# Kernel tuning notes

Hardware: AMD Instinct MI355X
Metric: run time of the kernel (lower is better)

## Reference

```python
import jax, jax.numpy as jnp
import numpy as np

N_EMBD = 768
N_HEAD = 12
HEAD_DIM = N_EMBD // N_HEAD  # 64


def apply_rotary_emb(x, cos, sin):
    d = x.shape[-1] // 2
    x1, x2 = x[..., :d], x[..., d:]
    y1 = x1 * cos + x2 * sin
    y2 = x1 * -sin + x2 * cos
    return jnp.concatenate([y1, y2], axis=-1)


def rms_norm(x):
    return x * jax.lax.rsqrt(jnp.mean(jnp.square(x), axis=-1, keepdims=True) + 1e-06)


def setup_inputs() -> dict:
    key = jax.random.key(0)
    ks = jax.random.split(key, 7)
    B, T = 2, 2048
    x = jax.random.normal(ks[0], (B, T, N_EMBD), dtype=jnp.float32)
    # cos/sin broadcast over (B, head) axes of [B, T, H, HEAD_DIM//2]
    cos = jax.random.uniform(ks[1], (T, 1, HEAD_DIM // 2), dtype=jnp.float32)
    sin = jax.random.uniform(ks[2], (T, 1, HEAD_DIM // 2), dtype=jnp.float32)
    scale = 1.0 / np.sqrt(N_EMBD)
    wq = jax.random.normal(ks[3], (N_EMBD, N_EMBD), dtype=jnp.float32) * scale
    wk = jax.random.normal(ks[4], (N_EMBD, N_EMBD), dtype=jnp.float32) * scale
    wv = jax.random.normal(ks[5], (N_EMBD, N_EMBD), dtype=jnp.float32) * scale
    wproj = jax.random.normal(ks[6], (N_EMBD, N_EMBD), dtype=jnp.float32) * scale
    return {"x": x, "cos": cos, "sin": sin, "wq": wq, "wk": wk, "wv": wv, "wproj": wproj}


def reference(x, cos, sin, wq, wk, wv, wproj):
    B, T, C = x.shape
    q = (x @ wq).reshape(B, T, N_HEAD, HEAD_DIM)
    k = (x @ wk).reshape(B, T, N_HEAD, HEAD_DIM)
    v = (x @ wv).reshape(B, T, N_HEAD, HEAD_DIM)
    q = rms_norm(apply_rotary_emb(q, cos, sin))
    k = rms_norm(apply_rotary_emb(k, cos, sin))
    # [B, H, T, T] attention scores (non-causal, as in source)
    attn = jnp.einsum('bqhd,bkhd->bhqk', q, k) / jnp.sqrt(jnp.float32(HEAD_DIM))
    attn = jax.nn.softmax(attn, axis=-1)
    y = jnp.einsum('bhqk,bkhd->bqhd', attn, v).reshape(B, T, C)
    return y @ wproj
```

## Files before the change

### kernel.cpp

```cpp
#include <hip/hip_runtime.h>
#include <hip/hip_bf16.h>
#include <stdint.h>

typedef __attribute__((ext_vector_type(8))) __bf16 bf16x8;
typedef __attribute__((ext_vector_type(4))) __bf16 bf16x4;
typedef __attribute__((ext_vector_type(4))) float f32x4;
typedef __attribute__((ext_vector_type(8))) unsigned short u16x8;

#define DEVI __device__ __forceinline__

DEVI void gload16(const void* g, void* l) {
  __builtin_amdgcn_global_load_lds((const __attribute__((address_space(1))) void*)g,
                                   (__attribute__((address_space(3))) void*)l, 16, 0, 0);
}

__global__ __launch_bounds__(256) void cvt_x_k(const float* __restrict__ x,
                                               __bf16* __restrict__ xb, int n4) {
  int i = blockIdx.x * blockDim.x + threadIdx.x;
  int stride = gridDim.x * blockDim.x;
  for (; i < n4; i += stride) {
    float4 v = ((const float4*)x)[i];
    bf16x4 o;
    o[0] = (__bf16)v.x; o[1] = (__bf16)v.y; o[2] = (__bf16)v.z; o[3] = (__bf16)v.w;
    ((bf16x4*)xb)[i] = o;
  }
}

__global__ __launch_bounds__(256) void wtrans_k(const float* __restrict__ wq,
                                                const float* __restrict__ wk,
                                                const float* __restrict__ wv,
                                                const float* __restrict__ wp,
                                                __bf16* __restrict__ WT) {
  __shared__ float tile[32][33];
  const float* W = (blockIdx.z == 0) ? wq : (blockIdx.z == 1) ? wk : (blockIdx.z == 2) ? wv : wp;
  int n0 = blockIdx.x * 32, k0 = blockIdx.y * 32;
  int tx = threadIdx.x, ty = threadIdx.y;
#pragma unroll
  for (int j = 0; j < 4; ++j)
    tile[ty + 8 * j][tx] = W[(size_t)(k0 + ty + 8 * j) * 768 + n0 + tx];
  __syncthreads();
#pragma unroll
  for (int j = 0; j < 4; ++j)
    WT[(size_t)(blockIdx.z * 768 + n0 + ty + 8 * j) * 768 + k0 + tx] =
        (__bf16)tile[tx][ty + 8 * j];
}

template <int EPI>
__global__ __launch_bounds__(256) void gemm_k(const __bf16* __restrict__ A,
                                              const __bf16* __restrict__ B,
                                              void* __restrict__ Cout,
                                              const float* __restrict__ cosT,
                                              const float* __restrict__ sinT,
                                              int K, int lda, int ldb, int ldc) {
  __shared__ __align__(16) __bf16 Al[128 * 32];
  __shared__ __align__(16) __bf16 Bl[128 * 32];
  const int tid = threadIdx.x, lane = tid & 63, w = tid >> 6;
  const int wm = w >> 1, wn = w & 1;
  const int m0 = blockIdx.y * 128, n0 = blockIdx.x * 128;
  const int c = lane & 15, g = lane >> 4;
  f32x4 acc[4][4] = {};

  for (int k0 = 0; k0 < K; k0 += 32) {
#pragma unroll
    for (int i = 0; i < 2; ++i) {
      int e = (i * 256 + tid) * 8;
      int row = e >> 5, col = e & 31;
      gload16(A + (size_t)(m0 + row) * lda + k0 + col, (char*)Al + 2 * (size_t)e);
      gload16(B + (size_t)(n0 + row) * ldb + k0 + col, (char*)Bl + 2 * (size_t)e);
    }
    __syncthreads();
    bf16x8 af[4], bfr[4];
#pragma unroll
    for (int q = 0; q < 4; ++q)
      af[q] = *(const bf16x8*)&Al[(wm * 64 + q * 16 + c) * 32 + 8 * g];
#pragma unroll
    for (int q = 0; q < 4; ++q)
      bfr[q] = *(const bf16x8*)&Bl[(wn * 64 + q * 16 + c) * 32 + 8 * g];
#pragma unroll
    for (int mf = 0; mf < 4; ++mf)
#pragma unroll
      for (int nf = 0; nf < 4; ++nf)
        acc[mf][nf] = __builtin_amdgcn_mfma_f32_16x16x32_bf16(af[mf], bfr[nf],
                                                              acc[mf][nf], 0, 0, 0);
    __syncthreads();
  }

  if (EPI == 1) {
    __bf16* out = (__bf16*)Cout;
    const int colbase = n0 + wn * 64;
    const int plane = colbase / 768;
#pragma unroll
    for (int mf = 0; mf < 4; ++mf) {
#pragma unroll
      for (int r = 0; r < 4; ++r) {
        int row = m0 + wm * 64 + mf * 16 + 4 * g + r;
        float v0 = acc[mf][0][r], v1 = acc[mf][1][r], v2 = acc[mf][2][r], v3 = acc[mf][3][r];
        float y0, y1, y2, y3;
        if (plane < 2) {
          int t = row & 2047;
          float c0 = cosT[t * 32 + c],      s0 = sinT[t * 32 + c];
          float c1 = cosT[t * 32 + 16 + c], s1 = sinT[t * 32 + 16 + c];
          y0 = v0 * c0 + v2 * s0;
          y2 = v2 * c0 - v0 * s0;
          y1 = v1 * c1 + v3 * s1;
          y3 = v3 * c1 - v1 * s1;
          float ss = y0 * y0 + y1 * y1 + y2 * y2 + y3 * y3;
          ss += __shfl_xor(ss, 1); ss += __shfl_xor(ss, 2);
          ss += __shfl_xor(ss, 4); ss += __shfl_xor(ss, 8);
          float rn = rsqrtf(ss * (1.0f / 64.0f) + 1e-6f);
          y0 *= rn; y1 *= rn; y2 *= rn; y3 *= rn;
        } else {
          y0 = v0; y1 = v1; y2 = v2; y3 = v3;
        }
        size_t base = (size_t)row * ldc + colbase + c;
        out[base +  0] = (__bf16)y0;
        out[base + 16] = (__bf16)y1;
        out[base + 32] = (__bf16)y2;
        out[base + 48] = (__bf16)y3;
      }
    }
  } else {
    float* out = (float*)Cout;
#pragma unroll
    for (int mf = 0; mf < 4; ++mf)
#pragma unroll
      for (int nf = 0; nf < 4; ++nf)
#pragma unroll
        for (int r = 0; r < 4; ++r) {
          int row = m0 + wm * 64 + mf * 16 + 4 * g + r;
          out[(size_t)row * ldc + n0 + wn * 64 + nf * 16 + c] = acc[mf][nf][r];
        }
  }
}

__global__ __launch_bounds__(256) void attn_k(const __bf16* __restrict__ QKV,
                                              __bf16* __restrict__ Yb) {
  constexpr int TT = 2048;
  __shared__ __align__(16) __bf16 Kl[128 * 64];
  __shared__ __align__(16) __bf16 Vl[64 * 128];
  __shared__ __align__(16) __bf16 Pl[4][16 * 136];
  const int tid = threadIdx.x, lane = tid & 63, w = tid >> 6;
  const int c = lane & 15, g = lane >> 4;
  const int qb = blockIdx.x, bh = blockIdx.y;
  const int b = bh / 12, h = bh % 12;
  const size_t ldq = 2304;
  const __bf16* Qg = QKV + (size_t)(b * TT) * ldq + h * 64;
  const __bf16* Kg = QKV + (size_t)(b * TT) * ldq + 768 + h * 64;
  const __bf16* Vg = QKV + (size_t)(b * TT) * ldq + 1536 + h * 64;

  bf16x8 aq0, aq1;
  {
    int row = qb * 64 + w * 16 + c;
    aq0 = *(const bf16x8*)(Qg + (size_t)row * ldq + 8 * g);
    aq1 = *(const bf16x8*)(Qg + (size_t)row * ldq + 32 + 8 * g);
  }

  f32x4 Yacc[4] = {};
  float m_run[4], l_run[4];
#pragma unroll
  for (int r = 0; r < 4; ++r) { m_run[r] = -__builtin_inff(); l_run[r] = 0.f; }

  for (int kv0 = 0; kv0 < TT; kv0 += 128) {
#pragma unroll
    for (int p = 0; p < 4; ++p) {
      int cid = p * 256 + tid;
      int row = cid >> 3, s = cid & 7;
      int srccol = 8 * (s ^ (row & 7));
      gload16(Kg + (size_t)(kv0 + row) * ldq + srccol, (char*)Kl + row * 128 + 16 * s);
    }
#pragma unroll
    for (int p = 0; p < 2; ++p) {
      int u = p * 256 + tid;
      int kp = u >> 3, d0 = (u & 7) * 8;
      const __bf16* src0 = Vg + (size_t)(kv0 + 2 * kp) * ldq + d0;
      u16x8 v0 = *(const u16x8*)src0;
      u16x8 v1 = *(const u16x8*)(src0 + ldq);
#pragma unroll
      for (int i = 0; i < 8; ++i) {
        int d = d0 + i;
        int byte = (d * 256 + 4 * kp) ^ ((d & 15) << 4);
        uint32_t pk = (uint32_t)v0[i] | ((uint32_t)v1[i] << 16);
        *(uint32_t*)((char*)Vl + byte) = pk;
      }
    }
    __syncthreads();

    f32x4 Sf[8];
    const f32x4 zero = {0.f, 0.f, 0.f, 0.f};
#pragma unroll
    for (int j = 0; j < 8; ++j) {
      int row = j * 16 + c;
      int sw = row & 7;
      bf16x8 bk0 = *(const bf16x8*)((char*)Kl + row * 128 + 16 * (g ^ sw));
      bf16x8 bk1 = *(const bf16x8*)((char*)Kl + row * 128 + 16 * ((g + 4) ^ sw));
      Sf[j] = __builtin_amdgcn_mfma_f32_16x16x32_bf16(aq0, bk0, zero, 0, 0, 0);
      Sf[j] = __builtin_amdgcn_mfma_f32_16x16x32_bf16(aq1, bk1, Sf[j], 0, 0, 0);
    }

#pragma unroll
    for (int r = 0; r < 4; ++r) {
      float mx = Sf[0][r];
#pragma unroll
      for (int j = 1; j < 8; ++j) mx = fmaxf(mx, Sf[j][r]);
      mx = fmaxf(mx, __shfl_xor(mx, 1));
      mx = fmaxf(mx, __shfl_xor(mx, 2));
      mx = fmaxf(mx, __shfl_xor(mx, 4));
      mx = fmaxf(mx, __shfl_xor(mx, 8));
      mx *= 0.125f;
      float mnew = fmaxf(m_run[r], mx);
      float corr = __expf(m_run[r] - mnew);
      float rs = 0.f;
#pragma unroll
      for (int j = 0; j < 8; ++j) {
        float p = __expf(Sf[j][r] * 0.125f - mnew);
        rs += p;
        Pl[w][(4 * g + r) * 136 + j * 16 + c] = (__bf16)p;
      }
      rs += __shfl_xor(rs, 1); rs += __shfl_xor(rs, 2);
      rs += __shfl_xor(rs, 4); rs += __shfl_xor(rs, 8);
      l_run[r] = l_run[r] * corr + rs;
      m_run[r] = mnew;
#pragma unroll
      for (int dn = 0; dn < 4; ++dn) Yacc[dn][r] *= corr;
    }
    __syncthreads();

#pragma unroll
    for (int kk = 0; kk < 4; ++kk) {
      bf16x8 ap = *(const bf16x8*)&Pl[w][c * 136 + kk * 32 + 8 * g];
#pragma unroll
      for (int dn = 0; dn < 4; ++dn) {
        int d = dn * 16 + c;
        int byte = (d * 256 + kk * 64 + 16 * g) ^ ((d & 15) << 4);
        bf16x8 bv = *(const bf16x8*)((char*)Vl + byte);
        Yacc[dn] = __builtin_amdgcn_mfma_f32_16x16x32_bf16(ap, bv, Yacc[dn], 0, 0, 0);
      }
    }
    __syncthreads();
  }

#pragma unroll
  for (int dn = 0; dn < 4; ++dn)
#pragma unroll
    for (int r = 0; r < 4; ++r) {
      float y = Yacc[dn][r] / l_run[r];
      int row = qb * 64 + w * 16 + 4 * g + r;
      Yb[(size_t)(b * TT + row) * 768 + h * 64 + dn * 16 + c] = (__bf16)y;
    }
}

extern "C" void kernel_launch(void* const* d_in, const int* in_sizes, int n_in,
                              void* d_out, int out_size, void* d_ws, size_t ws_size,
                              hipStream_t stream) {
  const float* x = (const float*)d_in[0];
  const float* cosT = (const float*)d_in[1];
  const float* sinT = (const float*)d_in[2];
  const float* wq = (const float*)d_in[3];
  const float* wk = (const float*)d_in[4];
  const float* wv = (const float*)d_in[5];
  const float* wp = (const float*)d_in[6];

  char* ws = (char*)d_ws;
  __bf16* xb   = (__bf16*)(ws);
  __bf16* WT   = (__bf16*)(ws + 6291456);
  __bf16* QKVb = (__bf16*)(ws + 11010048);
  __bf16* Yb   = (__bf16*)(ws + 29884416);

  cvt_x_k<<<2048, 256, 0, stream>>>(x, xb, (4096 * 768) / 4);
  wtrans_k<<<dim3(24, 24, 4), dim3(32, 8), 0, stream>>>(wq, wk, wv, wp, WT);
  gemm_k<1><<<dim3(18, 32), 256, 0, stream>>>(xb, WT, (void*)QKVb, cosT, sinT,
                                              768, 768, 768, 2304);
  attn_k<<<dim3(32, 24), 256, 0, stream>>>(QKVb, Yb);
  gemm_k<0><<<dim3(6, 32), 256, 0, stream>>>(Yb, WT + (size_t)2304 * 768, d_out,
                                             nullptr, nullptr, 768, 768, 768, 768);
}
```

Baseline: 222.1 us.

## Rework attention to 32x32 MFMA with register-resident P and coalesced output

The attention kernel now handles 128 queries per block (32 per wave) using 32x32x16 bf16 MFMA. It computes S^T so that each lane holds one query row's scores, which lets the softmax max and sum be done mostly in registers with a single cross-half shuffle. P is kept in registers and rearranged with lane shuffles instead of going through shared memory, which also removes one barrier per KV tile. Output goes through shared memory so global stores are coalesced. The projection GEMM is templated on BN and launched with 64-wide N tiles to put more blocks on the device; the cost is much higher register pressure in attention (64 floats of P plus 32 accumulators) under launch bounds of 2 blocks per SM.

Result: faster. 202.5 us (-8.9%).

```diff
diff --git a/kernel.cpp b/kernel.cpp
--- a/kernel.cpp
+++ b/kernel.cpp
@@ -4,14 +4,24 @@
 
 typedef __attribute__((ext_vector_type(8))) __bf16 bf16x8;
 typedef __attribute__((ext_vector_type(4))) __bf16 bf16x4;
+typedef __attribute__((ext_vector_type(2))) __bf16 bf16x2;
 typedef __attribute__((ext_vector_type(4))) float f32x4;
+typedef __attribute__((ext_vector_type(16))) float f32x16;
 typedef __attribute__((ext_vector_type(8))) unsigned short u16x8;
+typedef __attribute__((ext_vector_type(4))) unsigned int u32x4;
 
 #define DEVI __device__ __forceinline__
 
 DEVI void gload16(const void* g, void* l) {
   __builtin_amdgcn_global_load_lds((const __attribute__((address_space(1))) void*)g,
                                    (__attribute__((address_space(3))) void*)l, 16, 0, 0);
+}
+
+DEVI uint32_t pack2(float a, float b) {
+  bf16x2 t;
+  t[0] = (__bf16)a;
+  t[1] = (__bf16)b;
+  return __builtin_bit_cast(uint32_t, t);
 }
 
 __global__ __launch_bounds__(256) void cvt_x_k(const float* __restrict__ x,
@@ -45,20 +55,21 @@
         (__bf16)tile[tx][ty + 8 * j];
 }
 
-template <int EPI>
+template <int EPI, int BN>
 __global__ __launch_bounds__(256) void gemm_k(const __bf16* __restrict__ A,
                                               const __bf16* __restrict__ B,
                                               void* __restrict__ Cout,
                                               const float* __restrict__ cosT,
                                               const float* __restrict__ sinT,
                                               int K, int lda, int ldb, int ldc) {
+  constexpr int NF = BN / 32;
   __shared__ __align__(16) __bf16 Al[128 * 32];
-  __shared__ __align__(16) __bf16 Bl[128 * 32];
+  __shared__ __align__(16) __bf16 Bl[BN * 32];
   const int tid = threadIdx.x, lane = tid & 63, w = tid >> 6;
   const int wm = w >> 1, wn = w & 1;
-  const int m0 = blockIdx.y * 128, n0 = blockIdx.x * 128;
+  const int m0 = blockIdx.y * 128, n0 = blockIdx.x * BN;
   const int c = lane & 15, g = lane >> 4;
-  f32x4 acc[4][4] = {};
+  f32x4 acc[4][NF] = {};
 
   for (int k0 = 0; k0 < K; k0 += 32) {
 #pragma unroll
@@ -66,20 +77,25 @@
       int e = (i * 256 + tid) * 8;
       int row = e >> 5, col = e & 31;
       gload16(A + (size_t)(m0 + row) * lda + k0 + col, (char*)Al + 2 * (size_t)e);
+    }
+#pragma unroll
+    for (int i = 0; i < BN / 64; ++i) {
+      int e = (i * 256 + tid) * 8;
+      int row = e >> 5, col = e & 31;
       gload16(B + (size_t)(n0 + row) * ldb + k0 + col, (char*)Bl + 2 * (size_t)e);
     }
     __syncthreads();
-    bf16x8 af[4], bfr[4];
+    bf16x8 af[4], bfr[NF];
 #pragma unroll
     for (int q = 0; q < 4; ++q)
       af[q] = *(const bf16x8*)&Al[(wm * 64 + q * 16 + c) * 32 + 8 * g];
 #pragma unroll
-    for (int q = 0; q < 4; ++q)
-      bfr[q] = *(const bf16x8*)&Bl[(wn * 64 + q * 16 + c) * 32 + 8 * g];
+    for (int q = 0; q < NF; ++q)
+      bfr[q] = *(const bf16x8*)&Bl[(wn * (BN / 2) + q * 16 + c) * 32 + 8 * g];
 #pragma unroll
     for (int mf = 0; mf < 4; ++mf)
 #pragma unroll
-      for (int nf = 0; nf < 4; ++nf)
+      for (int nf = 0; nf < NF; ++nf)
         acc[mf][nf] = __builtin_amdgcn_mfma_f32_16x16x32_bf16(af[mf], bfr[nf],
                                                               acc[mf][nf], 0, 0, 0);
     __syncthreads();
@@ -124,41 +140,37 @@
 #pragma unroll
     for (int mf = 0; mf < 4; ++mf)
 #pragma unroll
-      for (int nf = 0; nf < 4; ++nf)
+      for (int nf = 0; nf < NF; ++nf)
 #pragma unroll
         for (int r = 0; r < 4; ++r) {
           int row = m0 + wm * 64 + mf * 16 + 4 * g + r;
-          out[(size_t)row * ldc + n0 + wn * 64 + nf * 16 + c] = acc[mf][nf][r];
+          out[(size_t)row * ldc + n0 + wn * (BN / 2) + nf * 16 + c] = acc[mf][nf][r];
         }
   }
 }
 
-__global__ __launch_bounds__(256) void attn_k(const __bf16* __restrict__ QKV,
-                                              __bf16* __restrict__ Yb) {
+__global__ __launch_bounds__(256, 2) void attn_k(const __bf16* __restrict__ QKV,
+                                                 __bf16* __restrict__ Yb) {
   constexpr int TT = 2048;
-  __shared__ __align__(16) __bf16 Kl[128 * 64];
-  __shared__ __align__(16) __bf16 Vl[64 * 128];
-  __shared__ __align__(16) __bf16 Pl[4][16 * 136];
+  __shared__ __align__(16) char smem[32768];
+  __bf16* Kl = (__bf16*)smem;
   const int tid = threadIdx.x, lane = tid & 63, w = tid >> 6;
-  const int c = lane & 15, g = lane >> 4;
+  const int q5 = lane & 31, h = lane >> 5;
   const int qb = blockIdx.x, bh = blockIdx.y;
-  const int b = bh / 12, h = bh % 12;
+  const int b = bh / 12, hd = bh % 12;
   const size_t ldq = 2304;
-  const __bf16* Qg = QKV + (size_t)(b * TT) * ldq + h * 64;
-  const __bf16* Kg = QKV + (size_t)(b * TT) * ldq + 768 + h * 64;
-  const __bf16* Vg = QKV + (size_t)(b * TT) * ldq + 1536 + h * 64;
-
-  bf16x8 aq0, aq1;
-  {
-    int row = qb * 64 + w * 16 + c;
-    aq0 = *(const bf16x8*)(Qg + (size_t)row * ldq + 8 * g);
-    aq1 = *(const bf16x8*)(Qg + (size_t)row * ldq + 32 + 8 * g);
-  }
-
-  f32x4 Yacc[4] = {};
-  float m_run[4], l_run[4];
-#pragma unroll
-  for (int r = 0; r < 4; ++r) { m_run[r] = -__builtin_inff(); l_run[r] = 0.f; }
+  const __bf16* Qg = QKV + (size_t)(b * TT) * ldq + hd * 64;
+  const __bf16* Kg = QKV + (size_t)(b * TT) * ldq + 768 + hd * 64;
+  const __bf16* Vg = QKV + (size_t)(b * TT) * ldq + 1536 + hd * 64;
+
+  const int qrow = qb * 128 + w * 32 + q5;
+  bf16x8 aq[4];
+#pragma unroll
+  for (int t = 0; t < 4; ++t)
+    aq[t] = *(const bf16x8*)(Qg + (size_t)qrow * ldq + t * 16 + 8 * h);
+
+  f32x16 Yacc[2] = {};
+  float m_run = -__builtin_inff(), l_run = 0.f;
 
   for (int kv0 = 0; kv0 < TT; kv0 += 128) {
 #pragma unroll
@@ -180,73 +192,99 @@
         int d = d0 + i;
         int byte = (d * 256 + 4 * kp) ^ ((d & 15) << 4);
         uint32_t pk = (uint32_t)v0[i] | ((uint32_t)v1[i] << 16);
-        *(uint32_t*)((char*)Vl + byte) = pk;
+        *(uint32_t*)(smem + 16384 + byte) = pk;
       }
     }
     __syncthreads();
 
-    f32x4 Sf[8];
-    const f32x4 zero = {0.f, 0.f, 0.f, 0.f};
-#pragma unroll
-    for (int j = 0; j < 8; ++j) {
-      int row = j * 16 + c;
-      int sw = row & 7;
-      bf16x8 bk0 = *(const bf16x8*)((char*)Kl + row * 128 + 16 * (g ^ sw));
-      bf16x8 bk1 = *(const bf16x8*)((char*)Kl + row * 128 + 16 * ((g + 4) ^ sw));
-      Sf[j] = __builtin_amdgcn_mfma_f32_16x16x32_bf16(aq0, bk0, zero, 0, 0, 0);
-      Sf[j] = __builtin_amdgcn_mfma_f32_16x16x32_bf16(aq1, bk1, Sf[j], 0, 0, 0);
-    }
-
-#pragma unroll
-    for (int r = 0; r < 4; ++r) {
-      float mx = Sf[0][r];
-#pragma unroll
-      for (int j = 1; j < 8; ++j) mx = fmaxf(mx, Sf[j][r]);
-      mx = fmaxf(mx, __shfl_xor(mx, 1));
-      mx = fmaxf(mx, __shfl_xor(mx, 2));
-      mx = fmaxf(mx, __shfl_xor(mx, 4));
-      mx = fmaxf(mx, __shfl_xor(mx, 8));
-      mx *= 0.125f;
-      float mnew = fmaxf(m_run[r], mx);
-      float corr = __expf(m_run[r] - mnew);
-      float rs = 0.f;
-#pragma unroll
-      for (int j = 0; j < 8; ++j) {
-        float p = __expf(Sf[j][r] * 0.125f - mnew);
-        rs += p;
-        Pl[w][(4 * g + r) * 136 + j * 16 + c] = (__bf16)p;
+    float p_[64];
+#pragma unroll
+    for (int j = 0; j < 4; ++j) {
+      f32x16 S = {};
+#pragma unroll
+      for (int t = 0; t < 4; ++t) {
+        int row = j * 32 + q5;
+        int chunk = (2 * t + h) ^ (q5 & 7);
+        bf16x8 kf = *(const bf16x8*)((char*)Kl + row * 128 + 16 * chunk);
+        S = __builtin_amdgcn_mfma_f32_32x32x16_bf16(kf, aq[t], S, 0, 0, 0);
       }
-      rs += __shfl_xor(rs, 1); rs += __shfl_xor(rs, 2);
-      rs += __shfl_xor(rs, 4); rs += __shfl_xor(rs, 8);
-      l_run[r] = l_run[r] * corr + rs;
-      m_run[r] = mnew;
-#pragma unroll
-      for (int dn = 0; dn < 4; ++dn) Yacc[dn][r] *= corr;
+#pragma unroll
+      for (int r = 0; r < 16; ++r) p_[j * 16 + r] = S[r];
+    }
+
+    float mx = p_[0];
+#pragma unroll
+    for (int i = 1; i < 64; ++i) mx = fmaxf(mx, p_[i]);
+    mx = fmaxf(mx, __shfl_xor(mx, 32));
+    float mnew = fmaxf(m_run, mx * 0.125f);
+    float corr = __expf(m_run - mnew);
+    float rs = 0.f;
+#pragma unroll
+    for (int i = 0; i < 64; ++i) {
+      float p = __expf(fmaf(p_[i], 0.125f, -mnew));
+      p_[i] = p;
+      rs += p;
+    }
+    rs += __shfl_xor(rs, 32);
+    l_run = l_run * corr + rs;
+    m_run = mnew;
+#pragma unroll
+    for (int dh = 0; dh < 2; ++dh)
+#pragma unroll
+      for (int r = 0; r < 16; ++r) Yacc[dh][r] *= corr;
+
+#pragma unroll
+    for (int j = 0; j < 4; ++j) {
+#pragma unroll
+      for (int s = 0; s < 2; ++s) {
+        const float* ps = p_ + j * 16 + s * 8;
+        uint32_t pk01 = pack2(ps[0], ps[1]);
+        uint32_t pk23 = pack2(ps[2], ps[3]);
+        uint32_t pk45 = pack2(ps[4], ps[5]);
+        uint32_t pk67 = pack2(ps[6], ps[7]);
+        uint32_t s01 = (uint32_t)__shfl_xor((int)pk01, 32);
+        uint32_t s23 = (uint32_t)__shfl_xor((int)pk23, 32);
+        uint32_t s45 = (uint32_t)__shfl_xor((int)pk45, 32);
+        uint32_t s67 = (uint32_t)__shfl_xor((int)pk67, 32);
+        u32x4 pw;
+        pw[0] = h ? s45 : pk01;
+        pw[1] = h ? s67 : pk23;
+        pw[2] = h ? pk45 : s01;
+        pw[3] = h ? pk67 : s23;
+        bf16x8 pfrag = __builtin_bit_cast(bf16x8, pw);
+        int keyb = j * 64 + s * 32 + 16 * h;
+#pragma unroll
+        for (int dh = 0; dh < 2; ++dh) {
+          int d = dh * 32 + q5;
+          int byte = (d * 256 + keyb) ^ ((d & 15) << 4);
+          bf16x8 vf = *(const bf16x8*)(smem + 16384 + byte);
+          Yacc[dh] = __builtin_amdgcn_mfma_f32_32x32x16_bf16(vf, pfrag, Yacc[dh], 0, 0, 0);
+        }
+      }
     }
     __syncthreads();
-
-#pragma unroll
-    for (int kk = 0; kk < 4; ++kk) {
-      bf16x8 ap = *(const bf16x8*)&Pl[w][c * 136 + kk * 32 + 8 * g];
-#pragma unroll
-      for (int dn = 0; dn < 4; ++dn) {
-        int d = dn * 16 + c;
-        int byte = (d * 256 + kk * 64 + 16 * g) ^ ((d & 15) << 4);
-        bf16x8 bv = *(const bf16x8*)((char*)Vl + byte);
-        Yacc[dn] = __builtin_amdgcn_mfma_f32_16x16x32_bf16(ap, bv, Yacc[dn], 0, 0, 0);
-      }
-    }
-    __syncthreads();
-  }
-
-#pragma unroll
-  for (int dn = 0; dn < 4; ++dn)
-#pragma unroll
-    for (int r = 0; r < 4; ++r) {
-      float y = Yacc[dn][r] / l_run[r];
-      int row = qb * 64 + w * 16 + 4 * g + r;
-      Yb[(size_t)(b * TT + row) * 768 + h * 64 + dn * 16 + c] = (__bf16)y;
-    }
+  }
+
+  float rl = __builtin_amdgcn_rcpf(l_run);
+  char* yb = smem + w * (32 * 144);
+#pragma unroll
+  for (int dh = 0; dh < 2; ++dh)
+#pragma unroll
+    for (int a = 0; a < 4; ++a) {
+      bf16x4 pkv;
+#pragma unroll
+      for (int i = 0; i < 4; ++i) pkv[i] = (__bf16)(Yacc[dh][a * 4 + i] * rl);
+      int d0 = a * 8 + 4 * h + 32 * dh;
+      *(bf16x4*)(yb + q5 * 144 + d0 * 2) = pkv;
+    }
+  __bf16* Yrow = Yb + (size_t)(b * TT + qb * 128 + w * 32) * 768 + hd * 64;
+#pragma unroll
+  for (int k = 0; k < 4; ++k) {
+    int chunk = k * 64 + lane;
+    int qr = chunk >> 3, sr = chunk & 7;
+    bf16x8 vv = *(const bf16x8*)(yb + qr * 144 + sr * 16);
+    *(bf16x8*)(Yrow + (size_t)qr * 768 + sr * 8) = vv;
+  }
 }
 
 extern "C" void kernel_launch(void* const* d_in, const int* in_sizes, int n_in,
@@ -268,9 +306,9 @@
 
   cvt_x_k<<<2048, 256, 0, stream>>>(x, xb, (4096 * 768) / 4);
   wtrans_k<<<dim3(24, 24, 4), dim3(32, 8), 0, stream>>>(wq, wk, wv, wp, WT);
-  gemm_k<1><<<dim3(18, 32), 256, 0, stream>>>(xb, WT, (void*)QKVb, cosT, sinT,
-                                              768, 768, 768, 2304);
-  attn_k<<<dim3(32, 24), 256, 0, stream>>>(QKVb, Yb);
-  gemm_k<0><<<dim3(6, 32), 256, 0, stream>>>(Yb, WT + (size_t)2304 * 768, d_out,
-                                             nullptr, nullptr, 768, 768, 768, 768);
-}
+  gemm_k<1, 128><<<dim3(18, 32), 256, 0, stream>>>(xb, WT, (void*)QKVb, cosT, sinT,
+                                                   768, 768, 768, 2304);
+  attn_k<<<dim3(16, 24), 256, 0, stream>>>(QKVb, Yb);
+  gemm_k<0, 64><<<dim3(12, 32), 256, 0, stream>>>(Yb, WT + (size_t)2304 * 768, d_out,
+                                                  nullptr, nullptr, 768, 768, 768, 768);
+}
```
